# Optimization experiments

Measured on AMD Instinct MI355X. Metric: run time of the kernel, lower is better.

Reference implementation:

```python
import jax, jax.numpy as jnp
import numpy as np

B, LQ, LKV, LT, C, H = 4, 1024, 1344, 320, 768, 12
DH = C // H
SCALE = DH ** -0.5
HID = 4 * C
EPS = 1e-5


def _ln(x, g, b):
    m = jnp.mean(x, axis=-1, keepdims=True)
    v = jnp.mean((x - m) ** 2, axis=-1, keepdims=True)
    return (x - m) * jax.lax.rsqrt(v + EPS) * g + b


def setup_inputs() -> dict:
    key = jax.random.key(0)
    ks = jax.random.split(key, 16)
    s = lambda k, shape, sc=0.02: jax.random.normal(k, shape, dtype=jnp.float32) * sc
    return {
        "tem_mask": s(ks[0], (B, LT, C), 1.0),
        "q": s(ks[1], (B, LQ, C), 1.0),
        "kv": s(ks[2], (B, LKV, C), 1.0),
        "attn_pos": s(ks[3], (1, H, LQ, LKV), 1.0),
        "ln1q_g": jnp.ones((C,)), "ln1q_b": jnp.zeros((C,)),
        "ln1kv_g": jnp.ones((C,)), "ln1kv_b": jnp.zeros((C,)),
        "Wq": s(ks[4], (C, C)), "bq": jnp.zeros((C,)),
        "Wkv": s(ks[5], (C, 2 * C)), "bkv": jnp.zeros((2 * C,)),
        "Wp": s(ks[6], (C, C)), "bp": jnp.zeros((C,)),
        "ln2_g": jnp.ones((C,)), "ln2_b": jnp.zeros((C,)),
        "W1": s(ks[7], (C, HID)), "b1": jnp.zeros((HID,)),
        "W2": s(ks[8], (HID, C)), "b2": jnp.zeros((C,)),
    }


def reference(tem_mask, q, kv, attn_pos, ln1q_g, ln1q_b, ln1kv_g, ln1kv_b,
              Wq, bq, Wkv, bkv, Wp, bp, ln2_g, ln2_b, W1, b1, W2, b2):
    qn = _ln(q, ln1q_g, ln1q_b)
    kvn = _ln(kv, ln1kv_g, ln1kv_b)
    # projections (attn_pos_encoding_only branch)
    qh = (qn @ Wq + bq).reshape(B, LQ, H, DH).transpose(0, 2, 1, 3)  # (B,H,Lq,Dh)
    kvp = kvn @ Wkv + bkv
    k, v = kvp[:, :, :C], kvp[:, :, C:]
    v = v.at[:, :LT, :].add(tem_mask)  # add template mask to template tokens
    kh = k.reshape(B, LKV, H, DH).transpose(0, 2, 1, 3)
    vh = v.reshape(B, LKV, H, DH).transpose(0, 2, 1, 3)
    attn = jnp.einsum('bhqd,bhkd->bhqk', qh, kh) * SCALE + attn_pos
    attn = jax.nn.softmax(attn, axis=-1)
    x = jnp.einsum('bhqk,bhkd->bhqd', attn, vh)
    x = x.transpose(0, 2, 1, 3).reshape(B, LQ, C)
    x = x @ Wp + bp
    q = q + x  # residual 1 (drop_path = Identity, dropout eval)
    h = _ln(q, ln2_g, ln2_b)
    h = jax.nn.gelu(h @ W1 + b1, approximate=False)
    h = h @ W2 + b2
    return q + h
```

## Files before the change

### kernel.cpp

```cpp
#include <hip/hip_runtime.h>
#include <hip/hip_bf16.h>
#include <math.h>

typedef __bf16 bf16x8 __attribute__((ext_vector_type(8)));
typedef float f32x4 __attribute__((ext_vector_type(4)));

__device__ __forceinline__ __hip_bfloat16 f2bf(float v){ return __float2bfloat16(v); }

__device__ __forceinline__ void gload16(const void* g, void* l){
  __builtin_amdgcn_global_load_lds(
      (const __attribute__((address_space(1))) void*)g,
      (__attribute__((address_space(3))) void*)l, 16, 0, 0);
}

__global__ void transpose_all(const float* __restrict__ Wq, const float* __restrict__ Wkv,
                              const float* __restrict__ Wp, const float* __restrict__ W1,
                              const float* __restrict__ W2,
                              __hip_bfloat16* __restrict__ oq, __hip_bfloat16* __restrict__ okv,
                              __hip_bfloat16* __restrict__ op_, __hip_bfloat16* __restrict__ o1,
                              __hip_bfloat16* __restrict__ o2){
  __shared__ float tile[32][33];
  const int bid = blockIdx.x;
  const float* in; __hip_bfloat16* out; int K, N, local;
  if(bid < 576)        { in=Wq;  out=oq;  K=768;  N=768;  local=bid; }
  else if(bid < 1728)  { in=Wkv; out=okv; K=768;  N=1536; local=bid-576; }
  else if(bid < 2304)  { in=Wp;  out=op_; K=768;  N=768;  local=bid-1728; }
  else if(bid < 4608)  { in=W1;  out=o1;  K=768;  N=3072; local=bid-2304; }
  else                 { in=W2;  out=o2;  K=3072; N=768;  local=bid-4608; }
  const int nbx = N/32;
  const int n0 = (local % nbx)*32, k0 = (local / nbx)*32;
  int tx = threadIdx.x, ty = threadIdx.y;
#pragma unroll
  for(int i=0;i<4;i++) tile[ty+i*8][tx] = in[(size_t)(k0+ty+i*8)*N + n0+tx];
  __syncthreads();
#pragma unroll
  for(int i=0;i<4;i++) out[(size_t)(n0+ty+i*8)*K + k0+tx] = f2bf(tile[tx][ty+i*8]);
}

__global__ __launch_bounds__(256) void transpose_vt(const __hip_bfloat16* __restrict__ vbuf,
                                                    __hip_bfloat16* __restrict__ vt){
  __shared__ __hip_bfloat16 tl[64][72];
  const int bh = blockIdx.x;
  const int kt = blockIdx.y;
  const int b = bh / 12, h = bh % 12;
  const int tid = threadIdx.x;
  const int r = tid >> 3, c = (tid & 7) * 8;
#pragma unroll
  for(int j=0;j<2;j++){
    uint4 v = *(const uint4*)(vbuf + ((size_t)(b*1344 + kt*64 + r + j*32))*768 + h*64 + c);
    *(uint4*)&tl[r + j*32][c] = v;
  }
  __syncthreads();
#pragma unroll
  for(int j=0;j<2;j++){
    int d = r + j*32;
    __hip_bfloat16 tmp[8];
#pragma unroll
    for(int i=0;i<8;i++) tmp[i] = tl[c + i][d];
    *(uint4*)(vt + ((size_t)(bh*64 + d))*1344 + kt*64 + c) = *(const uint4*)tmp;
  }
}

__device__ __forceinline__ void ln_body(const float* rp, const float* g, const float* b,
                                        __hip_bfloat16* op, int t){
  float x0 = rp[t], x1 = rp[t+256], x2 = rp[t+512];
  float s = x0+x1+x2, ss = x0*x0+x1*x1+x2*x2;
#pragma unroll
  for(int o=32;o>0;o>>=1){ s += __shfl_down(s,o); ss += __shfl_down(ss,o); }
  __shared__ float red[10];
  if((t&63)==0){ red[t>>6]=s; red[4+(t>>6)]=ss; }
  __syncthreads();
  if(t==0){
    float S=red[0]+red[1]+red[2]+red[3], SS=red[4]+red[5]+red[6]+red[7];
    float m=S*(1.f/768.f);
    red[8]=m; red[9]=SS*(1.f/768.f)-m*m;
  }
  __syncthreads();
  float m=red[8], r=rsqrtf(red[9]+1e-5f);
  op[t]     = f2bf((x0-m)*r*g[t]     + b[t]);
  op[t+256] = f2bf((x1-m)*r*g[t+256] + b[t+256]);
  op[t+512] = f2bf((x2-m)*r*g[t+512] + b[t+512]);
}

__global__ __launch_bounds__(256) void ln_qkv(const float* __restrict__ q, const float* __restrict__ kv,
    const float* __restrict__ qg, const float* __restrict__ qb,
    const float* __restrict__ kg, const float* __restrict__ kb2,
    __hip_bfloat16* __restrict__ qn, __hip_bfloat16* __restrict__ kvn){
  int row = blockIdx.x, t = threadIdx.x;
  if(row < 4096) ln_body(q + (size_t)row*768, qg, qb, qn + (size_t)row*768, t);
  else { row -= 4096; ln_body(kv + (size_t)row*768, kg, kb2, kvn + (size_t)row*768, t); }
}

__global__ __launch_bounds__(256) void ln_kernel(const float* __restrict__ in,
    const float* __restrict__ g, const float* __restrict__ b,
    __hip_bfloat16* __restrict__ out){
  int row = blockIdx.x, t = threadIdx.x;
  ln_body(in + (size_t)row*768, g, b, out + (size_t)row*768, t);
}

template<int BM, int BN, int EPI>
__global__ __launch_bounds__(256) void gemm_gl(
    const __hip_bfloat16* __restrict__ A, const __hip_bfloat16* __restrict__ BT,
    const float* __restrict__ bias, int M, int N, int K,
    void* __restrict__ out, const void* __restrict__ aux0, void* __restrict__ out2){
  constexpr int WR = (BM==128 || BN==64) ? 2 : 1;
  constexpr int WC = 4/WR;
  constexpr int MF = BM/(WR*16);
  constexpr int NF = BN/(WC*16);
  __shared__ char sA[2][BM*128];
  __shared__ char sB[2][BN*128];
  const int tid = threadIdx.x;
  const int l = tid & 63, w = tid >> 6;
  const int lg = l >> 4, li = l & 15;
  const int wrow = (WR==2) ? (w>>1)*(BM/2) : 0;
  const int wcol = (WC==2) ? (w&1)*(BN/2) : w*(BN/4);
  const int bm = blockIdx.x * BM;
  const int bn = blockIdx.y * BN;
  const int arow = w*(BM/4) + (l>>3);
  const int brow = w*(BN/4) + (l>>3);
  const int scol = ((((l&7)*16) ^ ((l>>3)<<4)) >> 1);

  auto stage = [&](int buf, int kt){
    const int k0 = kt*64;
#pragma unroll
    for(int i=0;i<BM/32;i++)
      gload16(A  + (size_t)(bm+arow+i*8)*K + k0 + scol, sA[buf] + (w*(BM/4))*128 + i*1024);
#pragma unroll
    for(int i=0;i<BN/32;i++)
      gload16(BT + (size_t)(bn+brow+i*8)*K + k0 + scol, sB[buf] + (w*(BN/4))*128 + i*1024);
  };

  f32x4 acc[MF][NF] = {};
  const int nk = K >> 6;
  stage(0, 0);
  __syncthreads();
  for(int kt=0; kt<nk; ++kt){
    const int cur = kt & 1;
    if(kt+1 < nk) stage(cur^1, kt+1);
#pragma unroll
    for(int kk=0;kk<2;kk++){
      const int kb = kk*64 + lg*16;
      bf16x8 af[MF], bfr[NF];
#pragma unroll
      for(int m=0;m<MF;m++){
        int row = wrow+m*16+li;
        af[m] = *(const bf16x8*)(sA[cur] + row*128 + (kb ^ ((row&7)<<4)));
      }
#pragma unroll
      for(int n=0;n<NF;n++){
        int row = wcol+n*16+li;
        bfr[n] = *(const bf16x8*)(sB[cur] + row*128 + (kb ^ ((row&7)<<4)));
      }
#pragma unroll
      for(int m=0;m<MF;m++)
#pragma unroll
        for(int n=0;n<NF;n++)
          acc[m][n] = __builtin_amdgcn_mfma_f32_16x16x32_bf16(af[m], bfr[n], acc[m][n],0,0,0);
    }
    __syncthreads();
  }
#pragma unroll
  for(int m=0;m<MF;m++){
#pragma unroll
    for(int n=0;n<NF;n++){
#pragma unroll
      for(int r=0;r<4;r++){
        int row = bm + wrow + m*16 + lg*4 + r;
        int col = bn + wcol + n*16 + li;
        float v = acc[m][n][r] + bias[col];
        if constexpr(EPI==0){
          ((__hip_bfloat16*)out)[(size_t)row*N + col] = f2bf(v * 0.125f);
        } else if constexpr(EPI==1){
          if(col < 768){
            ((__hip_bfloat16*)out)[(size_t)row*768 + col] = f2bf(v);
          } else {
            int c = col - 768;
            int bb = row / 1344, ii = row % 1344;
            if(ii < 320) v += ((const float*)aux0)[((size_t)bb*320 + ii)*768 + c];
            ((__hip_bfloat16*)out2)[(size_t)row*768 + c] = f2bf(v);
          }
        } else if constexpr(EPI==2){
          v += ((const float*)aux0)[(size_t)row*N + col];
          ((float*)out)[(size_t)row*N + col] = v;
        } else if constexpr(EPI==3){
          float u = v*(0.7978845608f + 0.0356774081f*v*v);
          float e = __expf(-2.f*fabsf(u));
          float th = (1.f - e)/(1.f + e);
          th = (u < 0.f) ? -th : th;
          ((__hip_bfloat16*)out)[(size_t)row*N + col] = f2bf(0.5f*v*(1.f+th));
        } else {
          v += ((const float*)aux0)[(size_t)row*N + col];
          ((float*)out)[(size_t)row*N + col] = v;
        }
      }
    }
  }
}

__global__ __launch_bounds__(256) void attn_kernel(
    const __hip_bfloat16* __restrict__ qh,
    const __hip_bfloat16* __restrict__ kb,
    const __hip_bfloat16* __restrict__ vt,
    const float* __restrict__ pos,
    __hip_bfloat16* __restrict__ xo){
  __shared__ char sK[2][8192];
  __shared__ char sV[2][8192];
  __shared__ char sP[4][2048];
  const int bid = blockIdx.x;
  const int qt = bid & 15, h = (bid >> 4) % 12, b = bid / 192;
  const int q0 = qt * 64;
  const int tid = threadIdx.x;
  const int l = tid & 63, w = tid >> 6;
  const int lg = l >> 4, li = l & 15;

  const int srow = w*16 + (l>>3);
  const int soff = (((l&7)*16) ^ ((l>>3)<<4)) >> 1;
  const __hip_bfloat16* ksrc = kb + ((size_t)b*1344 + srow)*768 + h*64 + soff;
  const __hip_bfloat16* vsrc = vt + ((size_t)(b*12+h)*64 + srow)*1344 + soff;

  bf16x8 aq[2];
  {
    const char* qp = (const char*)(qh + ((size_t)(b*1024 + q0 + w*16 + li))*768 + h*64);
    aq[0] = *(const bf16x8*)(qp + lg*16);
    aq[1] = *(const bf16x8*)(qp + 64 + lg*16);
  }
  const size_t posbase = ((size_t)h*1024 + q0 + w*16 + lg*4)*1344 + li;

  f32x4 accO[4] = {};
  float mrun[4], lrun[4];
#pragma unroll
  for(int r=0;r<4;r++){ mrun[r] = -1e30f; lrun[r] = 0.f; }

  auto stage = [&](int buf, int t){
    const size_t ko = (size_t)t*64*768;
    const size_t vo = (size_t)t*64;
    gload16(ksrc + ko,          sK[buf] + w*2048);
    gload16(ksrc + ko + 8*768,  sK[buf] + w*2048 + 1024);
    gload16(vsrc + vo,          sV[buf] + w*2048);
    gload16(vsrc + vo + 8*1344, sV[buf] + w*2048 + 1024);
  };
  auto ldpos = [&](int t, float (&pr)[4][4]){
    const float* pp = pos + posbase + (size_t)t*64;
#pragma unroll
    for(int n=0;n<4;n++)
#pragma unroll
      for(int r=0;r<4;r++)
        pr[n][r] = __builtin_nontemporal_load(pp + (size_t)r*1344 + n*16);
  };

  float pA[4][4], pB[4][4];
  ldpos(0, pA);
  stage(0, 0);
  __syncthreads();

  char* sPw = sP[w];

  auto body = [&](int t, float (&posr)[4][4], float (&npos)[4][4]){
    const int cur = t & 1;
    const bool more = (t < 20);
    f32x4 accS[4] = {};
    __builtin_amdgcn_s_setprio(1);
#pragma unroll
    for(int kk=0; kk<2; ++kk){
      const int kbyte = kk*64 + lg*16;
#pragma unroll
      for(int n=0;n<4;n++){
        int row = n*16 + li;
        bf16x8 bkf = *(const bf16x8*)(sK[cur] + row*128 + (kbyte ^ ((row&7)<<4)));
        accS[n] = __builtin_amdgcn_mfma_f32_16x16x32_bf16(aq[kk], bkf, accS[n], 0,0,0);
      }
    }
    __builtin_amdgcn_s_setprio(0);
    if(more) stage(cur^1, t+1);
    asm volatile("" ::: "memory");
    if(more) ldpos(t+1, npos);

    float p[4][4], mt[4];
#pragma unroll
    for(int r=0;r<4;r++) mt[r] = -1e30f;
#pragma unroll
    for(int n=0;n<4;n++)
#pragma unroll
      for(int r=0;r<4;r++){
        float s = accS[n][r] + posr[n][r];
        p[n][r] = s;
        mt[r] = fmaxf(mt[r], s);
      }
#pragma unroll
    for(int r=0;r<4;r++)
#pragma unroll
      for(int o=1;o<16;o<<=1) mt[r] = fmaxf(mt[r], __shfl_xor(mt[r], o));
    bool need = false;
#pragma unroll
    for(int r=0;r<4;r++) need |= (mt[r] > mrun[r] + 8.f);
    if(__any(need)){
#pragma unroll
      for(int r=0;r<4;r++){
        float mnew = fmaxf(mrun[r], mt[r]);
        float sf = __expf(mrun[r]-mnew);
        mrun[r] = mnew;
        lrun[r] *= sf;
#pragma unroll
        for(int n=0;n<4;n++) accO[n][r] *= sf;
      }
    }
#pragma unroll
    for(int r=0;r<4;r++){
      float rs = 0.f;
#pragma unroll
      for(int n=0;n<4;n++){ p[n][r] = __expf(p[n][r]-mrun[r]); rs += p[n][r]; }
#pragma unroll
      for(int o=1;o<16;o<<=1) rs += __shfl_xor(rs, o);
      lrun[r] += rs;
    }
#pragma unroll
    for(int n=0;n<4;n++)
#pragma unroll
      for(int r=0;r<4;r++){
        int qi = lg*4 + r, kj = n*16 + li;
        *(__hip_bfloat16*)(sPw + qi*128 + ((kj*2) ^ ((qi&7)<<4))) = f2bf(p[n][r]);
      }
    __builtin_amdgcn_s_setprio(1);
#pragma unroll
    for(int kk=0; kk<2; ++kk){
      const int kbyte = kk*64 + lg*16;
      bf16x8 pa = *(const bf16x8*)(sPw + li*128 + (kbyte ^ ((li&7)<<4)));
#pragma unroll
      for(int n=0;n<4;n++){
        int d = n*16 + li;
        bf16x8 bvf = *(const bf16x8*)(sV[cur] + d*128 + (kbyte ^ ((d&7)<<4)));
        accO[n] = __builtin_amdgcn_mfma_f32_16x16x32_bf16(pa, bvf, accO[n], 0,0,0);
      }
    }
    __builtin_amdgcn_s_setprio(0);
    if(more){
      asm volatile("s_waitcnt vmcnt(16)" ::: "memory");
      __builtin_amdgcn_s_barrier();
    }
  };

  for(int tt=0; tt<10; ++tt){
    body(2*tt,   pA, pB);
    body(2*tt+1, pB, pA);
  }
  body(20, pA, pB);

#pragma unroll
  for(int n=0;n<4;n++)
#pragma unroll
    for(int r=0;r<4;r++){
      int row = b*1024 + q0 + w*16 + lg*4 + r;
      int col = h*64 + n*16 + li;
      xo[(size_t)row*768 + col] = f2bf(accO[n][r] / lrun[r]);
    }
}

extern "C" void kernel_launch(void* const* d_in, const int* in_sizes, int n_in,
                              void* d_out, int out_size, void* d_ws, size_t ws_size,
                              hipStream_t stream){
  const float* tem   = (const float*)d_in[0];
  const float* qin   = (const float*)d_in[1];
  const float* kvin  = (const float*)d_in[2];
  const float* pos   = (const float*)d_in[3];
  const float* ln1qg = (const float*)d_in[4];
  const float* ln1qb = (const float*)d_in[5];
  const float* ln1kg = (const float*)d_in[6];
  const float* ln1kb = (const float*)d_in[7];
  const float* Wq    = (const float*)d_in[8];
  const float* bq    = (const float*)d_in[9];
  const float* Wkv   = (const float*)d_in[10];
  const float* bkv   = (const float*)d_in[11];
  const float* Wp    = (const float*)d_in[12];
  const float* bp    = (const float*)d_in[13];
  const float* ln2g  = (const float*)d_in[14];
  const float* ln2b  = (const float*)d_in[15];
  const float* W1    = (const float*)d_in[16];
  const float* b1    = (const float*)d_in[17];
  const float* W2    = (const float*)d_in[18];
  const float* b2    = (const float*)d_in[19];

  char* ws = (char*)d_ws; size_t off = 0;
  auto alloc = [&](size_t n){ char* p = ws + off; off = (off + n + 255) & ~(size_t)255; return p; };
  __hip_bfloat16* WqT  = (__hip_bfloat16*)alloc((size_t)768*768*2);
  __hip_bfloat16* WkvT = (__hip_bfloat16*)alloc((size_t)1536*768*2);
  __hip_bfloat16* WpT  = (__hip_bfloat16*)alloc((size_t)768*768*2);
  __hip_bfloat16* W1T  = (__hip_bfloat16*)alloc((size_t)3072*768*2);
  __hip_bfloat16* W2T  = (__hip_bfloat16*)alloc((size_t)768*3072*2);
  __hip_bfloat16* qn   = (__hip_bfloat16*)alloc((size_t)4096*768*2);
  char* poolBase = alloc((size_t)5376*768*2*3 + (size_t)4096*768*2);
  __hip_bfloat16* kvn  = (__hip_bfloat16*)poolBase;
  __hip_bfloat16* kbuf = kvn  + (size_t)5376*768;
  __hip_bfloat16* vbuf = kbuf + (size_t)5376*768;
  __hip_bfloat16* qhb  = vbuf + (size_t)5376*768;
  __hip_bfloat16* xat  = (__hip_bfloat16*)alloc((size_t)4096*768*2);
  float*          x1f  = (float*)alloc((size_t)4096*768*4);
  __hip_bfloat16* vt   = kvn;
  __hip_bfloat16* hln  = qn;
  __hip_bfloat16* h1   = kvn;

  transpose_all<<<6912, dim3(32,8), 0, stream>>>(Wq, Wkv, Wp, W1, W2, WqT, WkvT, WpT, W1T, W2T);
  ln_qkv<<<4096+5376, 256, 0, stream>>>(qin, kvin, ln1qg, ln1qb, ln1kg, ln1kb, qn, kvn);

  gemm_gl<64,64,0>  <<<dim3(64, 12), 256, 0, stream>>>(qn,  WqT,  bq,  4096, 768,  768,  qhb, nullptr, nullptr);
  gemm_gl<128,128,1><<<dim3(42, 12), 256, 0, stream>>>(kvn, WkvT, bkv, 5376, 1536, 768,  kbuf, tem, vbuf);
  transpose_vt<<<dim3(48, 21), 256, 0, stream>>>(vbuf, vt);

  attn_kernel<<<768, 256, 0, stream>>>(qhb, kbuf, vt, pos, xat);

  gemm_gl<64,64,2>  <<<dim3(64, 12), 256, 0, stream>>>(xat, WpT,  bp,  4096, 768,  768,  x1f, qin, nullptr);
  ln_kernel<<<4096, 256, 0, stream>>>(x1f, ln2g, ln2b, hln);
  gemm_gl<128,128,3><<<dim3(32, 24), 256, 0, stream>>>(hln, W1T,  b1,  4096, 3072, 768,  h1, nullptr, nullptr);
  gemm_gl<64,64,4>  <<<dim3(64, 12), 256, 0, stream>>>(h1,  W2T,  b2,  4096, 768,  3072, (float*)d_out, x1f, nullptr);
}
```

Measured before the change: 237.6 us.

## Fuse V transpose into KV GEMM epilogue and compute softmax row sums via MFMA

The KV projection GEMM epilogue now writes V directly in the transposed per-head layout (d-major, token-minor) with packed 4-element stores, which removes the separate transpose_vt kernel and its extra read/write pass over V. In the attention kernel, the per-row softmax denominator is no longer built with a shuffle reduction. It is accumulated by an extra MFMA against a ones vector on the bf16 probabilities. This cuts cross-lane reductions but sums the rounded bf16 probabilities, which slightly changes the numerics, and the transposed-V epilogue stores are strided.

```diff
diff --git a/kernel.cpp b/kernel.cpp
--- a/kernel.cpp
+++ b/kernel.cpp
@@ -35,30 +35,6 @@
   __syncthreads();
 #pragma unroll
   for(int i=0;i<4;i++) out[(size_t)(n0+ty+i*8)*K + k0+tx] = f2bf(tile[tx][ty+i*8]);
-}
-
-__global__ __launch_bounds__(256) void transpose_vt(const __hip_bfloat16* __restrict__ vbuf,
-                                                    __hip_bfloat16* __restrict__ vt){
-  __shared__ __hip_bfloat16 tl[64][72];
-  const int bh = blockIdx.x;
-  const int kt = blockIdx.y;
-  const int b = bh / 12, h = bh % 12;
-  const int tid = threadIdx.x;
-  const int r = tid >> 3, c = (tid & 7) * 8;
-#pragma unroll
-  for(int j=0;j<2;j++){
-    uint4 v = *(const uint4*)(vbuf + ((size_t)(b*1344 + kt*64 + r + j*32))*768 + h*64 + c);
-    *(uint4*)&tl[r + j*32][c] = v;
-  }
-  __syncthreads();
-#pragma unroll
-  for(int j=0;j<2;j++){
-    int d = r + j*32;
-    __hip_bfloat16 tmp[8];
-#pragma unroll
-    for(int i=0;i<8;i++) tmp[i] = tl[c + i][d];
-    *(uint4*)(vt + ((size_t)(bh*64 + d))*1344 + kt*64 + c) = *(const uint4*)tmp;
-  }
 }
 
 __device__ __forceinline__ void ln_body(const float* rp, const float* g, const float* b,
@@ -163,34 +139,46 @@
   for(int m=0;m<MF;m++){
 #pragma unroll
     for(int n=0;n<NF;n++){
-#pragma unroll
-      for(int r=0;r<4;r++){
-        int row = bm + wrow + m*16 + lg*4 + r;
-        int col = bn + wcol + n*16 + li;
-        float v = acc[m][n][r] + bias[col];
-        if constexpr(EPI==0){
-          ((__hip_bfloat16*)out)[(size_t)row*N + col] = f2bf(v * 0.125f);
-        } else if constexpr(EPI==1){
-          if(col < 768){
-            ((__hip_bfloat16*)out)[(size_t)row*768 + col] = f2bf(v);
+      if constexpr(EPI==1){
+        const int col = bn + wcol + n*16 + li;
+        const int row0 = bm + wrow + m*16 + lg*4;
+        const int bb = row0 / 1344, ii = row0 % 1344;
+        if(col < 768){
+#pragma unroll
+          for(int r=0;r<4;r++)
+            ((__hip_bfloat16*)out)[(size_t)(row0+r)*768 + col] = f2bf(acc[m][n][r] + bias[col]);
+        } else {
+          const int c = col - 768, hh = c >> 6, d = c & 63;
+          __hip_bfloat16 tmp[4];
+#pragma unroll
+          for(int r=0;r<4;r++){
+            float v = acc[m][n][r] + bias[col];
+            if(ii < 320) v += ((const float*)aux0)[((size_t)bb*320 + ii + r)*768 + c];
+            tmp[r] = f2bf(v);
+          }
+          *(uint2*)((__hip_bfloat16*)out2 + ((size_t)(bb*12+hh)*64 + d)*1344 + ii) = *(const uint2*)tmp;
+        }
+      } else {
+#pragma unroll
+        for(int r=0;r<4;r++){
+          int row = bm + wrow + m*16 + lg*4 + r;
+          int col = bn + wcol + n*16 + li;
+          float v = acc[m][n][r] + bias[col];
+          if constexpr(EPI==0){
+            ((__hip_bfloat16*)out)[(size_t)row*N + col] = f2bf(v * 0.125f);
+          } else if constexpr(EPI==2){
+            v += ((const float*)aux0)[(size_t)row*N + col];
+            ((float*)out)[(size_t)row*N + col] = v;
+          } else if constexpr(EPI==3){
+            float u = v*(0.7978845608f + 0.0356774081f*v*v);
+            float e = __expf(-2.f*fabsf(u));
+            float th = (1.f - e)/(1.f + e);
+            th = (u < 0.f) ? -th : th;
+            ((__hip_bfloat16*)out)[(size_t)row*N + col] = f2bf(0.5f*v*(1.f+th));
           } else {
-            int c = col - 768;
-            int bb = row / 1344, ii = row % 1344;
-            if(ii < 320) v += ((const float*)aux0)[((size_t)bb*320 + ii)*768 + c];
-            ((__hip_bfloat16*)out2)[(size_t)row*768 + c] = f2bf(v);
+            v += ((const float*)aux0)[(size_t)row*N + col];
+            ((float*)out)[(size_t)row*N + col] = v;
           }
-        } else if constexpr(EPI==2){
-          v += ((const float*)aux0)[(size_t)row*N + col];
-          ((float*)out)[(size_t)row*N + col] = v;
-        } else if constexpr(EPI==3){
-          float u = v*(0.7978845608f + 0.0356774081f*v*v);
-          float e = __expf(-2.f*fabsf(u));
-          float th = (1.f - e)/(1.f + e);
-          th = (u < 0.f) ? -th : th;
-          ((__hip_bfloat16*)out)[(size_t)row*N + col] = f2bf(0.5f*v*(1.f+th));
-        } else {
-          v += ((const float*)aux0)[(size_t)row*N + col];
-          ((float*)out)[(size_t)row*N + col] = v;
         }
       }
     }
@@ -224,12 +212,16 @@
     aq[0] = *(const bf16x8*)(qp + lg*16);
     aq[1] = *(const bf16x8*)(qp + 64 + lg*16);
   }
+  bf16x8 ones;
+#pragma unroll
+  for(int i=0;i<8;i++) ones[i] = (__bf16)1.0f;
   const size_t posbase = ((size_t)h*1024 + q0 + w*16 + lg*4)*1344 + li;
 
   f32x4 accO[4] = {};
-  float mrun[4], lrun[4];
-#pragma unroll
-  for(int r=0;r<4;r++){ mrun[r] = -1e30f; lrun[r] = 0.f; }
+  f32x4 accL = {};
+  float mrun[4];
+#pragma unroll
+  for(int r=0;r<4;r++) mrun[r] = -1e30f;
 
   auto stage = [&](int buf, int t){
     const size_t ko = (size_t)t*64*768;
@@ -299,20 +291,15 @@
         float mnew = fmaxf(mrun[r], mt[r]);
         float sf = __expf(mrun[r]-mnew);
         mrun[r] = mnew;
-        lrun[r] *= sf;
+        accL[r] *= sf;
 #pragma unroll
         for(int n=0;n<4;n++) accO[n][r] *= sf;
       }
     }
 #pragma unroll
-    for(int r=0;r<4;r++){
-      float rs = 0.f;
-#pragma unroll
-      for(int n=0;n<4;n++){ p[n][r] = __expf(p[n][r]-mrun[r]); rs += p[n][r]; }
-#pragma unroll
-      for(int o=1;o<16;o<<=1) rs += __shfl_xor(rs, o);
-      lrun[r] += rs;
-    }
+    for(int n=0;n<4;n++)
+#pragma unroll
+      for(int r=0;r<4;r++) p[n][r] = __expf(p[n][r]-mrun[r]);
 #pragma unroll
     for(int n=0;n<4;n++)
 #pragma unroll
@@ -325,6 +312,7 @@
     for(int kk=0; kk<2; ++kk){
       const int kbyte = kk*64 + lg*16;
       bf16x8 pa = *(const bf16x8*)(sPw + li*128 + (kbyte ^ ((li&7)<<4)));
+      accL = __builtin_amdgcn_mfma_f32_16x16x32_bf16(pa, ones, accL, 0,0,0);
 #pragma unroll
       for(int n=0;n<4;n++){
         int d = n*16 + li;
@@ -351,7 +339,7 @@
     for(int r=0;r<4;r++){
       int row = b*1024 + q0 + w*16 + lg*4 + r;
       int col = h*64 + n*16 + li;
-      xo[(size_t)row*768 + col] = f2bf(accO[n][r] / lrun[r]);
+      xo[(size_t)row*768 + col] = f2bf(accO[n][r] / accL[r]);
     }
 }
 
@@ -390,11 +378,10 @@
   char* poolBase = alloc((size_t)5376*768*2*3 + (size_t)4096*768*2);
   __hip_bfloat16* kvn  = (__hip_bfloat16*)poolBase;
   __hip_bfloat16* kbuf = kvn  + (size_t)5376*768;
-  __hip_bfloat16* vbuf = kbuf + (size_t)5376*768;
-  __hip_bfloat16* qhb  = vbuf + (size_t)5376*768;
+  __hip_bfloat16* vt   = kbuf + (size_t)5376*768;
+  __hip_bfloat16* qhb  = vt   + (size_t)5376*768;
   __hip_bfloat16* xat  = (__hip_bfloat16*)alloc((size_t)4096*768*2);
   float*          x1f  = (float*)alloc((size_t)4096*768*4);
-  __hip_bfloat16* vt   = kvn;
   __hip_bfloat16* hln  = qn;
   __hip_bfloat16* h1   = kvn;
 
@@ -402,8 +389,7 @@
   ln_qkv<<<4096+5376, 256, 0, stream>>>(qin, kvin, ln1qg, ln1qb, ln1kg, ln1kb, qn, kvn);
 
   gemm_gl<64,64,0>  <<<dim3(64, 12), 256, 0, stream>>>(qn,  WqT,  bq,  4096, 768,  768,  qhb, nullptr, nullptr);
-  gemm_gl<128,128,1><<<dim3(42, 12), 256, 0, stream>>>(kvn, WkvT, bkv, 5376, 1536, 768,  kbuf, tem, vbuf);
-  transpose_vt<<<dim3(48, 21), 256, 0, stream>>>(vbuf, vt);
+  gemm_gl<128,128,1><<<dim3(42, 12), 256, 0, stream>>>(kvn, WkvT, bkv, 5376, 1536, 768,  kbuf, tem, vt);
 
   attn_kernel<<<768, 256, 0, stream>>>(qhb, kbuf, vt, pos, xat);
 
```

Measured after the change: 223.1 us. 6.1% less time.
